# Kernel optimization log

Hardware: AMD Instinct MI355X
Metric: run time of the kernel (lower is better)

The kernel has to match this reference:

```python
import jax, jax.numpy as jnp
import numpy as np

B, S_WP, D_BERT = 64, 512, 768
NUM_WORDS = 256   # max words per sentence (segment count for scatter-mean)
H = 256           # LSTM hidden dim
A_MAX, K_MAX = 8, 4
N_LABELS = 4


def setup_inputs() -> dict:
    key = jax.random.key(0)
    ks = jax.random.split(key, 16)
    s = lambda shape, k, scale=0.05: jax.random.normal(k, shape, jnp.float32) * scale
    inp = {
        "embeddings": jax.random.normal(ks[0], (B, S_WP, D_BERT), jnp.float32),
        "mask": jnp.sort(jax.random.randint(ks[1], (B, S_WP), 0, NUM_WORDS), axis=-1),
        "aspect_idxs": jax.random.randint(ks[2], (B, A_MAX, K_MAX), 0, NUM_WORDS - 2),
        "w_ih_f": s((4 * H, D_BERT), ks[3]),
        "w_hh_f": s((4 * H, H), ks[4]),
        "b_ih_f": s((4 * H,), ks[5]),
        "b_hh_f": s((4 * H,), ks[6]),
        "w_ih_r": s((4 * H, D_BERT), ks[7]),
        "w_hh_r": s((4 * H, H), ks[8]),
        "b_ih_r": s((4 * H,), ks[9]),
        "b_hh_r": s((4 * H,), ks[10]),
        "fc1_w": s((H, 4 * H), ks[11]),
        "fc1_b": s((H,), ks[12]),
        "fc2_w": s((N_LABELS, H), ks[13]),
        "fc2_b": s((N_LABELS,), ks[14]),
    }
    return inp


def _lstm_dir(x, w_ih, w_hh, b_ih, b_hh, reverse):
    # x: [B, S, D] -> [B, S, H]; PyTorch gate order i, f, g, o.
    b, _, _ = x.shape
    h_dim = w_hh.shape[1]
    xg = jnp.einsum('bsd,gd->bsg', x, w_ih) + b_ih  # precompute input gates

    def step(carry, xg_t):
        h, c = carry
        g = xg_t + h @ w_hh.T + b_hh
        i, f, gg, o = jnp.split(g, 4, axis=-1)
        c = jax.nn.sigmoid(f) * c + jax.nn.sigmoid(i) * jnp.tanh(gg)
        h = jax.nn.sigmoid(o) * jnp.tanh(c)
        return (h, c), h

    init = (jnp.zeros((b, h_dim), x.dtype), jnp.zeros((b, h_dim), x.dtype))
    _, hs = jax.lax.scan(step, init, xg.transpose(1, 0, 2), reverse=reverse)
    return hs.transpose(1, 0, 2)


def _forward(embeddings, mask, aspect_idxs, w_ih_f, w_hh_f, b_ih_f, b_hh_f,
             w_ih_r, w_hh_r, b_ih_r, b_hh_r, fc1_w, fc1_b, fc2_w, fc2_b):
    # batch_scatter_mean: pool wordpieces into words via segment mean.
    seg_sum = jax.vmap(lambda e, m: jax.ops.segment_sum(e, m, num_segments=NUM_WORDS))(embeddings, mask)
    cnt = jax.vmap(lambda m: jax.ops.segment_sum(jnp.ones(m.shape, embeddings.dtype), m, num_segments=NUM_WORDS))(mask)
    words = seg_sum / jnp.maximum(cnt, 1.0)[..., None]  # [B, NUM_WORDS, D_BERT]

    # Bidirectional LSTM (dropout is identity in eval).
    h_f = _lstm_dir(words, w_ih_f, w_hh_f, b_ih_f, b_hh_f, reverse=False)
    h_r = _lstm_dir(words, w_ih_r, w_hh_r, b_ih_r, b_hh_r, reverse=True)
    out = jnp.concatenate([h_f, h_r], axis=-1)  # [B, S_words, 2H]

    b, s, hd = out.shape
    sent_mean = out.mean(axis=1)  # [B, 2H] (mean over full padded sequence, as original)

    # Ragged aspect gather-mean: sent_out[idxs + 1].mean(0), -1 pads masked out.
    tok_valid = (aspect_idxs >= 0).astype(out.dtype)              # [B, A, K]
    idx = jnp.clip(aspect_idxs, 0, s - 2) + 1                     # [B, A, K]
    gathered = jnp.take_along_axis(out, idx.reshape(b, -1, 1), axis=1)  # [B, A*K, 2H]
    gathered = gathered.reshape(b, A_MAX, K_MAX, hd)
    n_tok = tok_valid.sum(-1)                                     # [B, A]
    asp_mean = (gathered * tok_valid[..., None]).sum(2) / jnp.maximum(n_tok, 1.0)[..., None]

    valid = (n_tok > 0)[..., None]
    sent_b = jnp.broadcast_to(sent_mean[:, None, :], (b, A_MAX, hd))
    emb = jnp.where(valid, jnp.concatenate([sent_b, asp_mean], axis=-1), 0.0)  # [B, A, 4H]

    flat = emb.reshape(b * A_MAX, 2 * hd)
    h1 = jax.nn.relu(flat @ fc1_w.T + fc1_b)
    logits = h1 @ fc2_w.T + fc2_b
    return logits.reshape(b, A_MAX, -1)


def reference(embeddings, mask, aspect_idxs, w_ih_f, w_hh_f, b_ih_f, b_hh_f,
              w_ih_r, w_hh_r, b_ih_r, b_hh_r, fc1_w, fc1_b, fc2_w, fc2_b):
    return _forward(embeddings, mask, aspect_idxs, w_ih_f, w_hh_f, b_ih_f, b_hh_f,
                    w_ih_r, w_hh_r, b_ih_r, b_hh_r, fc1_w, fc1_b, fc2_w, fc2_b)
```

## Files before the change

### kernel.cpp

```cpp
#include <hip/hip_runtime.h>
#include <hip/hip_bf16.h>
#include <hip/hip_fp16.h>

#define B_   64
#define SWP  512
#define D_   768
#define W_   256
#define H_   256
#define G4   1024
#define N2   2048
#define M_   16384
#define A_   8
#define KK_  4

typedef __attribute__((ext_vector_type(4))) float f32x4;
typedef __attribute__((ext_vector_type(8))) short bf16x8;
typedef _Float16 __attribute__((ext_vector_type(2))) h2_t;

#define KR2 96
#define KT2 32

__device__ __forceinline__ void gload_lds16(const void* g, void* l) {
  __builtin_amdgcn_global_load_lds((const __attribute__((address_space(1))) void*)g,
                                   (__attribute__((address_space(3))) void*)l, 16, 0, 0);
}

__device__ __forceinline__ float sigm(float x) { return 1.f / (1.f + __expf(-x)); }
__device__ __forceinline__ float tanh_(float x) { return 1.f - 2.f / (1.f + __expf(2.f * x)); }

__device__ __forceinline__ float dot2acc(h2_t w, h2_t h, float acc) {
#if __has_builtin(__builtin_amdgcn_fdot2)
  return __builtin_amdgcn_fdot2(w, h, acc, false);
#else
  return acc + (float)w[0] * (float)h[0] + (float)w[1] * (float)h[1];
#endif
}

__device__ __forceinline__ h2_t bc_h2(unsigned int v) {
  union { unsigned int u; h2_t h; } cvt;
  cvt.u = v;
  return cvt.h;
}

__global__ __launch_bounds__(256) void k_words(const float* __restrict__ emb,
                                               const int* __restrict__ mask,
                                               __hip_bfloat16* __restrict__ words) {
  const int b = blockIdx.x >> 8;
  const int w = blockIdx.x & 255;
  const int tid = threadIdx.x;
  __shared__ int m[SWP];
  m[tid] = mask[b * SWP + tid];
  m[tid + 256] = mask[b * SWP + 256 + tid];
  __syncthreads();
  int lo = 0, hi = SWP;
  while (lo < hi) { int mid = (lo + hi) >> 1; if (m[mid] < w) lo = mid + 1; else hi = mid; }
  int lo2 = lo, hi2 = SWP;
  while (lo2 < hi2) { int mid = (lo2 + hi2) >> 1; if (m[mid] < w + 1) lo2 = mid + 1; else hi2 = mid; }
  const int cnt = lo2 - lo;
  const float inv = (cnt > 0) ? 1.f / (float)cnt : 0.f;
  float s0 = 0.f, s1 = 0.f, s2 = 0.f;
  for (int s = lo; s < lo2; ++s) {
    const float* row = emb + ((size_t)b * SWP + s) * D_;
    s0 += row[tid]; s1 += row[tid + 256]; s2 += row[tid + 512];
  }
  __hip_bfloat16* o = words + ((size_t)b * W_ + w) * D_;
  o[tid]       = __float2bfloat16(s0 * inv);
  o[tid + 256] = __float2bfloat16(s1 * inv);
  o[tid + 512] = __float2bfloat16(s2 * inv);
}

__global__ __launch_bounds__(256) void k_prep_wih(const float* __restrict__ wf, const float* __restrict__ wr,
                                                  const float* __restrict__ bihf, const float* __restrict__ bhhf,
                                                  const float* __restrict__ bihr, const float* __restrict__ bhhr,
                                                  __hip_bfloat16* __restrict__ wih, float* __restrict__ bias) {
  const int i = blockIdx.x * 256 + threadIdx.x;
  const int n = i / D_;
  const int k = i - n * D_;
  const float v = (n < G4) ? wf[n * D_ + k] : wr[(n - G4) * D_ + k];
  wih[i] = __float2bfloat16(v);
  if (i < N2) {
    bias[i] = (i < G4) ? (bihf[i] + bhhf[i]) : (bihr[i - G4] + bhhr[i - G4]);
  }
}

__global__ __launch_bounds__(256) void k_prep_whh(const float* __restrict__ whf,
                                                  const float* __restrict__ whr,
                                                  h2_t* __restrict__ whhP) {
  const int i = blockIdx.x * 256 + threadIdx.x;
  const int d = i >> 17;
  const int kk = (i >> 10) & 127;
  const int r = i & 1023;
  const float* w = d ? whr : whf;
  h2_t v;
  v[0] = (_Float16)w[r * H_ + 2 * kk];
  v[1] = (_Float16)w[r * H_ + 2 * kk + 1];
  whhP[i] = v;
}

__global__ __launch_bounds__(256) void k_gemm_xg(const __hip_bfloat16* __restrict__ A,
                                                 const __hip_bfloat16* __restrict__ Wt,
                                                 const float* __restrict__ bias,
                                                 _Float16* __restrict__ C) {
  const int bm = blockIdx.y * 128;
  const int bn = blockIdx.x * 128;
  __shared__ __hip_bfloat16 As[128 * 32];
  __shared__ __hip_bfloat16 Bs[128 * 32];
  const int tid = threadIdx.x;
  const int lane = tid & 63;
  const int wave = tid >> 6;
  const int wm = (wave >> 1) * 64;
  const int wn = (wave & 1) * 64;
  const int l15 = lane & 15;
  const int l4 = lane >> 4;
  const int row_a = tid >> 2;
  const int chunk = tid & 3;
  f32x4 acc[4][4] = {};
  for (int k0 = 0; k0 < D_; k0 += 32) {
    const __hip_bfloat16* ga  = A  + (size_t)(bm + row_a) * D_ + k0 + chunk * 8;
    const __hip_bfloat16* ga2 = A  + (size_t)(bm + 64 + row_a) * D_ + k0 + chunk * 8;
    const __hip_bfloat16* gb  = Wt + (size_t)(bn + row_a) * D_ + k0 + chunk * 8;
    const __hip_bfloat16* gb2 = Wt + (size_t)(bn + 64 + row_a) * D_ + k0 + chunk * 8;
    gload_lds16(ga,  As + tid * 8);
    gload_lds16(ga2, As + 2048 + tid * 8);
    gload_lds16(gb,  Bs + tid * 8);
    gload_lds16(gb2, Bs + 2048 + tid * 8);
    __syncthreads();
    bf16x8 af[4], bf[4];
#pragma unroll
    for (int i = 0; i < 4; ++i) {
      af[i] = *(const bf16x8*)(As + (wm + i * 16 + l15) * 32 + l4 * 8);
      bf[i] = *(const bf16x8*)(Bs + (wn + i * 16 + l15) * 32 + l4 * 8);
    }
#pragma unroll
    for (int i = 0; i < 4; ++i)
#pragma unroll
      for (int j = 0; j < 4; ++j)
        acc[i][j] = __builtin_amdgcn_mfma_f32_16x16x32_bf16(af[i], bf[j], acc[i][j], 0, 0, 0);
    __syncthreads();
  }
#pragma unroll
  for (int i = 0; i < 4; ++i) {
    const int m = bm + wm + i * 16 + l4 * 4;
#pragma unroll
    for (int j = 0; j < 4; ++j) {
      const int n = bn + wn + j * 16 + l15;
      const float bs = bias[n];
#pragma unroll
      for (int r = 0; r < 4; ++r)
        C[(size_t)(m + r) * N2 + n] = (_Float16)(acc[i][j][r] + bs);
    }
  }
}

__global__ __launch_bounds__(1024)
void k_lstm(const _Float16* __restrict__ xg,
            const h2_t* __restrict__ whhP,
            float* __restrict__ out) {
  const int bx = blockIdx.x;
  const int d = bx & 1;
  const int b = bx >> 1;
  const int t = threadIdx.x;
  const int u = t & 255;
  const int gate = t >> 8;
  const int l = t & 63;

  __shared__ __align__(16) _Float16 hbuf[2][256];
  __shared__ __align__(16) h2_t wtail[8][1024][4];
  __shared__ float gbuf[3][256];

  const h2_t* wp = whhP + (size_t)d * (128 * 1024);
  h2_t wreg[KR2];
#pragma unroll
  for (int kk = 0; kk < KR2; ++kk) wreg[kk] = wp[kk * 1024 + t];
#pragma unroll
  for (int c = 0; c < 8; ++c) {
#pragma unroll
    for (int j = 0; j < 4; ++j)
      wtail[c][t][j] = wp[(KR2 + c * 4 + j) * 1024 + t];
  }
  if (t < 256) hbuf[0][t] = (_Float16)0.f;
  __syncthreads();

  float c_state = 0.f;
  for (int step = 0; step < W_; ++step) {
    const int tt = d ? (W_ - 1 - step) : step;
    const float xv = (float)xg[((size_t)b * W_ + tt) * N2 + d * G4 + t];
    const unsigned int hA = *(const unsigned int*)&hbuf[step & 1][2 * l];
    const unsigned int hB = *(const unsigned int*)&hbuf[step & 1][128 + 2 * l];
    float a = 0.f, a2 = 0.f;
#pragma unroll
    for (int kk = 0; kk < 64; kk += 2) {
      a  = dot2acc(wreg[kk],     bc_h2(__builtin_amdgcn_readlane(hA, kk)),     a);
      a2 = dot2acc(wreg[kk + 1], bc_h2(__builtin_amdgcn_readlane(hA, kk + 1)), a2);
    }
#pragma unroll
    for (int kk = 64; kk < KR2; kk += 2) {
      a  = dot2acc(wreg[kk],     bc_h2(__builtin_amdgcn_readlane(hB, kk - 64)),     a);
      a2 = dot2acc(wreg[kk + 1], bc_h2(__builtin_amdgcn_readlane(hB, kk - 63)), a2);
    }
#pragma unroll
    for (int c = 0; c < 8; ++c) {
      const f32x4 wv = *(const f32x4*)&wtail[c][t][0];
      const h2_t* wvp = (const h2_t*)&wv;
      a  = dot2acc(wvp[0], bc_h2(__builtin_amdgcn_readlane(hB, 32 + c * 4 + 0)), a);
      a2 = dot2acc(wvp[1], bc_h2(__builtin_amdgcn_readlane(hB, 32 + c * 4 + 1)), a2);
      a  = dot2acc(wvp[2], bc_h2(__builtin_amdgcn_readlane(hB, 32 + c * 4 + 2)), a);
      a2 = dot2acc(wvp[3], bc_h2(__builtin_amdgcn_readlane(hB, 32 + c * 4 + 3)), a2);
    }
    const float av = a + a2 + xv;
    if (gate != 0) gbuf[gate - 1][u] = av;
    __syncthreads();
    if (gate == 0) {
      const float ig = sigm(av);
      const float fg = sigm(gbuf[0][u]);
      const float gg = tanh_(gbuf[1][u]);
      const float og = sigm(gbuf[2][u]);
      c_state = fg * c_state + ig * gg;
      const float h = og * tanh_(c_state);
      out[((size_t)b * W_ + tt) * 512 + d * 256 + u] = h;
      hbuf[(step + 1) & 1][u] = (_Float16)h;
    }
    __syncthreads();
  }
}

__global__ __launch_bounds__(256) void k_head(const float* __restrict__ out,
                                              const int* __restrict__ aidx,
                                              const float* __restrict__ fc1w,
                                              const float* __restrict__ fc1b,
                                              const float* __restrict__ fc2w,
                                              const float* __restrict__ fc2b,
                                              float* __restrict__ logits) {
  const int b = blockIdx.x;
  const int t = threadIdx.x;
  __shared__ float emb[A_][1024];
  __shared__ float h1[A_][256];
  __shared__ float sent[512];
  const float* ob = out + (size_t)b * W_ * 512;
  float s0 = 0.f, s1 = 0.f;
  for (int tt = 0; tt < W_; ++tt) {
    s0 += ob[tt * 512 + t];
    s1 += ob[tt * 512 + 256 + t];
  }
  sent[t] = s0 * (1.f / 256.f);
  sent[t + 256] = s1 * (1.f / 256.f);
  __syncthreads();
  for (int a = 0; a < A_; ++a) {
    int nv = 0;
    float m0 = 0.f, m1 = 0.f;
    for (int k = 0; k < KK_; ++k) {
      const int idx = aidx[(b * A_ + a) * KK_ + k];
      if (idx >= 0) {
        const int tt = min(idx, W_ - 2) + 1;
        m0 += ob[tt * 512 + t];
        m1 += ob[tt * 512 + 256 + t];
        nv++;
      }
    }
    const float inv = nv > 0 ? 1.f / (float)nv : 0.f;
    const bool valid = nv > 0;
    emb[a][t]        = valid ? sent[t] : 0.f;
    emb[a][t + 256]  = valid ? sent[t + 256] : 0.f;
    emb[a][512 + t]       = m0 * inv;
    emb[a][512 + 256 + t] = m1 * inv;
  }
  __syncthreads();
  {
    float acc[A_];
#pragma unroll
    for (int a = 0; a < A_; ++a) acc[a] = fc1b[t];
    const float* wrow = fc1w + (size_t)t * 1024;
    for (int j = 0; j < 1024; j += 4) {
      const float4 w = *(const float4*)(wrow + j);
#pragma unroll
      for (int a = 0; a < A_; ++a) {
        const float4 e = *(const float4*)(&emb[a][j]);
        acc[a] += w.x * e.x + w.y * e.y + w.z * e.z + w.w * e.w;
      }
    }
#pragma unroll
    for (int a = 0; a < A_; ++a) h1[a][t] = fmaxf(acc[a], 0.f);
  }
  __syncthreads();
  if (t < A_ * 4) {
    const int a = t >> 2, l = t & 3;
    float acc = fc2b[l];
    const float* w = fc2w + l * 256;
    for (int j = 0; j < 256; ++j) acc += w[j] * h1[a][j];
    logits[(b * A_ + a) * 4 + l] = acc;
  }
}

extern "C" void kernel_launch(void* const* d_in, const int* in_sizes, int n_in,
                              void* d_out, int out_size, void* d_ws, size_t ws_size,
                              hipStream_t stream) {
  const float* emb  = (const float*)d_in[0];
  const int*   mask = (const int*)d_in[1];
  const int*   aidx = (const int*)d_in[2];
  const float* wihf = (const float*)d_in[3];
  const float* whhf = (const float*)d_in[4];
  const float* bihf = (const float*)d_in[5];
  const float* bhhf = (const float*)d_in[6];
  const float* wihr = (const float*)d_in[7];
  const float* whhr = (const float*)d_in[8];
  const float* bihr = (const float*)d_in[9];
  const float* bhhr = (const float*)d_in[10];
  const float* fc1w = (const float*)d_in[11];
  const float* fc1b = (const float*)d_in[12];
  const float* fc2w = (const float*)d_in[13];
  const float* fc2b = (const float*)d_in[14];
  float* logits = (float*)d_out;

  char* ws = (char*)d_ws;
  size_t off = 0;
  auto alloc = [&](size_t bytes) -> void* {
    void* p = ws + off;
    off += (bytes + 255) & ~(size_t)255;
    return p;
  };
  __hip_bfloat16* words = (__hip_bfloat16*)alloc((size_t)M_ * D_ * 2);
  _Float16*       xg    = (_Float16*)alloc((size_t)M_ * N2 * 2);
  __hip_bfloat16* wih   = (__hip_bfloat16*)alloc((size_t)N2 * D_ * 2);
  float*          bias  = (float*)alloc((size_t)N2 * 4);
  h2_t*           whhP  = (h2_t*)alloc((size_t)2 * 128 * 1024 * 4);
  float*          outh  = (float*)alloc((size_t)B_ * W_ * 512 * 4);

  k_words<<<B_ * W_, 256, 0, stream>>>(emb, mask, words);
  k_prep_wih<<<(N2 * D_) / 256, 256, 0, stream>>>(wihf, wihr, bihf, bhhf, bihr, bhhr, wih, bias);
  k_prep_whh<<<(2 * 128 * 1024) / 256, 256, 0, stream>>>(whhf, whhr, whhP);
  dim3 gg(N2 / 128, M_ / 128);
  k_gemm_xg<<<gg, 256, 0, stream>>>(words, wih, bias, xg);
  k_lstm<<<B_ * 2, 1024, 0, stream>>>(xg, whhP, outh);
  k_head<<<B_, 256, 0, stream>>>(outh, aidx, fc1w, fc1b, fc2w, fc2b, logits);
}
```

Baseline: 746.1 us.

## Compute all four LSTM gates per thread in 256-thread blocks

The LSTM recurrence kernel moves from 1024 threads (one gate per thread) to 256 threads, each computing all four gates for one hidden unit. This removes the gate-exchange shared buffer and one barrier per step. Hidden state is now read as vectors from LDS instead of broadcast with readlane, and the next step's input gates are prefetched. In exchange each thread holds 384 packed weight registers at one wave per EU, so spilling and reduced latency hiding are risks.

```diff
diff --git a/kernel.cpp b/kernel.cpp
--- a/kernel.cpp
+++ b/kernel.cpp
@@ -34,12 +34,6 @@
 #else
   return acc + (float)w[0] * (float)h[0] + (float)w[1] * (float)h[1];
 #endif
-}
-
-__device__ __forceinline__ h2_t bc_h2(unsigned int v) {
-  union { unsigned int u; h2_t h; } cvt;
-  cvt.u = v;
-  return cvt.h;
 }
 
 __global__ __launch_bounds__(256) void k_words(const float* __restrict__ emb,
@@ -152,7 +146,8 @@
   }
 }
 
-__global__ __launch_bounds__(1024)
+__global__ __launch_bounds__(256)
+__attribute__((amdgpu_waves_per_eu(1, 1)))
 void k_lstm(const _Float16* __restrict__ xg,
             const h2_t* __restrict__ whhP,
             float* __restrict__ out) {
@@ -160,67 +155,97 @@
   const int d = bx & 1;
   const int b = bx >> 1;
   const int t = threadIdx.x;
-  const int u = t & 255;
-  const int gate = t >> 8;
-  const int l = t & 63;
 
   __shared__ __align__(16) _Float16 hbuf[2][256];
-  __shared__ __align__(16) h2_t wtail[8][1024][4];
-  __shared__ float gbuf[3][256];
+  __shared__ __align__(16) h2_t wtail[32][256][4];
 
   const h2_t* wp = whhP + (size_t)d * (128 * 1024);
-  h2_t wreg[KR2];
-#pragma unroll
-  for (int kk = 0; kk < KR2; ++kk) wreg[kk] = wp[kk * 1024 + t];
-#pragma unroll
-  for (int c = 0; c < 8; ++c) {
-#pragma unroll
-    for (int j = 0; j < 4; ++j)
-      wtail[c][t][j] = wp[(KR2 + c * 4 + j) * 1024 + t];
-  }
-  if (t < 256) hbuf[0][t] = (_Float16)0.f;
-  __syncthreads();
+
+  h2_t wI[KR2], wF[KR2], wG[KR2], wO[KR2];
+#pragma unroll 96
+  for (int kk = 0; kk < KR2; ++kk) {
+    wI[kk] = wp[kk * 1024 + t];
+    wF[kk] = wp[kk * 1024 + 256 + t];
+    wG[kk] = wp[kk * 1024 + 512 + t];
+    wO[kk] = wp[kk * 1024 + 768 + t];
+  }
+#pragma unroll
+  for (int c = 0; c < 32; ++c) {
+    const int g = c >> 3, j = c & 7;
+    f32x4 v;
+#pragma unroll
+    for (int q = 0; q < 4; ++q) {
+      h2_t w = wp[(KR2 + j * 4 + q) * 1024 + g * 256 + t];
+      ((h2_t*)&v)[q] = w;
+    }
+    *(f32x4*)&wtail[c][t][0] = v;
+  }
+  hbuf[0][t] = (_Float16)0.f;
+  __syncthreads();
+
+  int tt = d ? (W_ - 1) : 0;
+  const _Float16* xr = xg + ((size_t)b * W_ + tt) * N2 + d * G4;
+  float xI = (float)xr[t], xF = (float)xr[256 + t];
+  float xG = (float)xr[512 + t], xO = (float)xr[768 + t];
 
   float c_state = 0.f;
   for (int step = 0; step < W_; ++step) {
-    const int tt = d ? (W_ - 1 - step) : step;
-    const float xv = (float)xg[((size_t)b * W_ + tt) * N2 + d * G4 + t];
-    const unsigned int hA = *(const unsigned int*)&hbuf[step & 1][2 * l];
-    const unsigned int hB = *(const unsigned int*)&hbuf[step & 1][128 + 2 * l];
-    float a = 0.f, a2 = 0.f;
-#pragma unroll
-    for (int kk = 0; kk < 64; kk += 2) {
-      a  = dot2acc(wreg[kk],     bc_h2(__builtin_amdgcn_readlane(hA, kk)),     a);
-      a2 = dot2acc(wreg[kk + 1], bc_h2(__builtin_amdgcn_readlane(hA, kk + 1)), a2);
-    }
-#pragma unroll
-    for (int kk = 64; kk < KR2; kk += 2) {
-      a  = dot2acc(wreg[kk],     bc_h2(__builtin_amdgcn_readlane(hB, kk - 64)),     a);
-      a2 = dot2acc(wreg[kk + 1], bc_h2(__builtin_amdgcn_readlane(hB, kk - 63)), a2);
-    }
-#pragma unroll
-    for (int c = 0; c < 8; ++c) {
-      const f32x4 wv = *(const f32x4*)&wtail[c][t][0];
-      const h2_t* wvp = (const h2_t*)&wv;
-      a  = dot2acc(wvp[0], bc_h2(__builtin_amdgcn_readlane(hB, 32 + c * 4 + 0)), a);
-      a2 = dot2acc(wvp[1], bc_h2(__builtin_amdgcn_readlane(hB, 32 + c * 4 + 1)), a2);
-      a  = dot2acc(wvp[2], bc_h2(__builtin_amdgcn_readlane(hB, 32 + c * 4 + 2)), a);
-      a2 = dot2acc(wvp[3], bc_h2(__builtin_amdgcn_readlane(hB, 32 + c * 4 + 3)), a2);
-    }
-    const float av = a + a2 + xv;
-    if (gate != 0) gbuf[gate - 1][u] = av;
+    const int cur = step & 1;
+    float nI = 0.f, nF = 0.f, nG = 0.f, nO = 0.f;
+    if (step + 1 < W_) {
+      const int tt1 = d ? (W_ - 2 - step) : (step + 1);
+      const _Float16* xr1 = xg + ((size_t)b * W_ + tt1) * N2 + d * G4;
+      nI = (float)xr1[t]; nF = (float)xr1[256 + t];
+      nG = (float)xr1[512 + t]; nO = (float)xr1[768 + t];
+    }
+
+    const f32x4* hb4 = (const f32x4*)&hbuf[cur][0];
+    float aI = 0.f, aF = 0.f, aG = 0.f, aO = 0.f;
+#pragma unroll
+    for (int c = 0; c < 24; ++c) {
+      const f32x4 hv = hb4[c];
+      const h2_t* hp = (const h2_t*)&hv;
+#pragma unroll
+      for (int q = 0; q < 4; ++q) {
+        aI = dot2acc(wI[c * 4 + q], hp[q], aI);
+        aF = dot2acc(wF[c * 4 + q], hp[q], aF);
+        aG = dot2acc(wG[c * 4 + q], hp[q], aG);
+        aO = dot2acc(wO[c * 4 + q], hp[q], aO);
+      }
+    }
+#pragma unroll
+    for (int j = 0; j < 8; ++j) {
+      const f32x4 hv = hb4[24 + j];
+      const h2_t* hp = (const h2_t*)&hv;
+      const f32x4 vI = *(const f32x4*)&wtail[j][t][0];
+      const f32x4 vF = *(const f32x4*)&wtail[8 + j][t][0];
+      const f32x4 vG = *(const f32x4*)&wtail[16 + j][t][0];
+      const f32x4 vO = *(const f32x4*)&wtail[24 + j][t][0];
+      const h2_t* pI = (const h2_t*)&vI;
+      const h2_t* pF = (const h2_t*)&vF;
+      const h2_t* pG = (const h2_t*)&vG;
+      const h2_t* pO = (const h2_t*)&vO;
+#pragma unroll
+      for (int q = 0; q < 4; ++q) {
+        aI = dot2acc(pI[q], hp[q], aI);
+        aF = dot2acc(pF[q], hp[q], aF);
+        aG = dot2acc(pG[q], hp[q], aG);
+        aO = dot2acc(pO[q], hp[q], aO);
+      }
+    }
+
+    const float ig = sigm(aI + xI);
+    const float fg = sigm(aF + xF);
+    const float gg = tanh_(aG + xG);
+    const float og = sigm(aO + xO);
+    c_state = fg * c_state + ig * gg;
+    const float h = og * tanh_(c_state);
+    out[((size_t)b * W_ + tt) * 512 + d * 256 + t] = h;
+    hbuf[cur ^ 1][t] = (_Float16)h;
     __syncthreads();
-    if (gate == 0) {
-      const float ig = sigm(av);
-      const float fg = sigm(gbuf[0][u]);
-      const float gg = tanh_(gbuf[1][u]);
-      const float og = sigm(gbuf[2][u]);
-      c_state = fg * c_state + ig * gg;
-      const float h = og * tanh_(c_state);
-      out[((size_t)b * W_ + tt) * 512 + d * 256 + u] = h;
-      hbuf[(step + 1) & 1][u] = (_Float16)h;
-    }
-    __syncthreads();
+
+    tt = d ? (W_ - 2 - step) : (step + 1);
+    xI = nI; xF = nF; xG = nG; xO = nO;
   }
 }
 
@@ -330,6 +355,6 @@
   k_prep_whh<<<(2 * 128 * 1024) / 256, 256, 0, stream>>>(whhf, whhr, whhP);
   dim3 gg(N2 / 128, M_ / 128);
   k_gemm_xg<<<gg, 256, 0, stream>>>(words, wih, bias, xg);
-  k_lstm<<<B_ * 2, 1024, 0, stream>>>(xg, whhP, outh);
+  k_lstm<<<B_ * 2, 256, 0, stream>>>(xg, whhP, outh);
   k_head<<<B_, 256, 0, stream>>>(outh, aidx, fc1w, fc1b, fc2w, fc2b, logits);
 }
```

Result: slower. 1.030 ms (+38.1%).

## Split each LSTM sequence across two workgroups with flag-based hidden-state exchange

Applied to the files above, without the earlier changes.

The recurrent LSTM kernel now uses two 512-thread workgroups per (batch, direction) pair, each owning half the hidden units. After every step the halves swap their fp16 hidden vectors through global memory, using release/acquire flags and spin-waiting. The recurrent weights are spread over registers, LDS and a pre-packed global stream that is reloaded every step. This doubles the number of CUs working on the serial recurrence, at the cost of a cross-workgroup handshake per timestep that assumes all 256 workgroups are co-resident.

```diff
diff --git a/kernel.cpp b/kernel.cpp
--- a/kernel.cpp
+++ b/kernel.cpp
@@ -17,8 +17,9 @@
 typedef __attribute__((ext_vector_type(8))) short bf16x8;
 typedef _Float16 __attribute__((ext_vector_type(2))) h2_t;
 
-#define KR2 96
-#define KT2 32
+#define PVC 32
+#define NLC 12
+#define NSC 12
 
 __device__ __forceinline__ void gload_lds16(const void* g, void* l) {
   __builtin_amdgcn_global_load_lds((const __attribute__((address_space(1))) void*)g,
@@ -95,6 +96,28 @@
   v[0] = (_Float16)w[r * H_ + 2 * kk];
   v[1] = (_Float16)w[r * H_ + 2 * kk + 1];
   whhP[i] = v;
+}
+
+__global__ __launch_bounds__(256) void k_prep_wstr(const h2_t* __restrict__ whhP,
+                                                   f32x4* __restrict__ wstr) {
+  const int i = blockIdx.x * 256 + threadIdx.x;
+  if (i >= 2 * 2 * NSC * 512) return;
+  const int t = i & 511;
+  const int c = (i >> 9) % NSC;
+  const int duh = i / (NSC * 512);
+  const int d = duh >> 1;
+  const int uh = duh & 1;
+  const int r = (t >> 7) * 256 + uh * 128 + (t & 127);
+  const h2_t* wp = whhP + (size_t)d * (128 * 1024);
+  f32x4 v;
+#pragma unroll
+  for (int q = 0; q < 4; ++q)
+    ((h2_t*)&v)[q] = wp[(80 + 4 * c + q) * 1024 + r];
+  wstr[i] = v;
+}
+
+__global__ __launch_bounds__(256) void k_zero_flags(int* __restrict__ flags) {
+  flags[threadIdx.x] = 0;
 }
 
 __global__ __launch_bounds__(256) void k_gemm_xg(const __hip_bfloat16* __restrict__ A,
@@ -152,75 +175,126 @@
   }
 }
 
-__global__ __launch_bounds__(1024)
+__global__ __launch_bounds__(512)
 void k_lstm(const _Float16* __restrict__ xg,
             const h2_t* __restrict__ whhP,
+            const f32x4* __restrict__ wstr,
+            unsigned* __restrict__ hx,
+            int* __restrict__ flags,
             float* __restrict__ out) {
-  const int bx = blockIdx.x;
-  const int d = bx & 1;
-  const int b = bx >> 1;
+  const int bid = blockIdx.x;
+  const int p = bid & 127;
+  const int uh = bid >> 7;
+  const int d = p & 1;
+  const int b = p >> 1;
   const int t = threadIdx.x;
-  const int u = t & 255;
-  const int gate = t >> 8;
+  const int g = t >> 7;
+  const int us = t & 127;
+  const int u = uh * 128 + us;
+  const int r = g * 256 + u;
   const int l = t & 63;
-
-  __shared__ __align__(16) _Float16 hbuf[2][256];
-  __shared__ __align__(16) h2_t wtail[8][1024][4];
-  __shared__ float gbuf[3][256];
+  const int myidx = p * 2 + uh;
+  const int paidx = p * 2 + (uh ^ 1);
+
+  __shared__ __align__(16) _Float16 hbuf[256];
+  __shared__ __align__(16) h2_t wlds[NLC][512][4];
+  __shared__ float gbuf[3][128];
 
   const h2_t* wp = whhP + (size_t)d * (128 * 1024);
-  h2_t wreg[KR2];
-#pragma unroll
-  for (int kk = 0; kk < KR2; ++kk) wreg[kk] = wp[kk * 1024 + t];
-#pragma unroll
-  for (int c = 0; c < 8; ++c) {
-#pragma unroll
-    for (int j = 0; j < 4; ++j)
-      wtail[c][t][j] = wp[(KR2 + c * 4 + j) * 1024 + t];
-  }
-  if (t < 256) hbuf[0][t] = (_Float16)0.f;
+  const f32x4* wsp = wstr + (size_t)(d * 2 + uh) * (NSC * 512);
+
+  unsigned wv[PVC];
+#pragma unroll
+  for (int j = 0; j < PVC; ++j)
+    wv[j] = *(const unsigned*)&wp[j * 1024 + r];
+#pragma unroll
+  for (int c = 0; c < NLC; ++c) {
+    f32x4 v;
+#pragma unroll
+    for (int q = 0; q < 4; ++q)
+      ((h2_t*)&v)[q] = wp[(PVC + 4 * c + q) * 1024 + r];
+    *(f32x4*)&wlds[c][t][0] = v;
+  }
+  if (t < 256) hbuf[t] = (_Float16)0.f;
   __syncthreads();
 
   float c_state = 0.f;
+#pragma unroll 1
   for (int step = 0; step < W_; ++step) {
     const int tt = d ? (W_ - 1 - step) : step;
-    const float xv = (float)xg[((size_t)b * W_ + tt) * N2 + d * G4 + t];
-    const unsigned int hA = *(const unsigned int*)&hbuf[step & 1][2 * l];
-    const unsigned int hB = *(const unsigned int*)&hbuf[step & 1][128 + 2 * l];
+    const float xv = (float)xg[((size_t)b * W_ + tt) * N2 + d * G4 + r];
     float a = 0.f, a2 = 0.f;
-#pragma unroll
-    for (int kk = 0; kk < 64; kk += 2) {
-      a  = dot2acc(wreg[kk],     bc_h2(__builtin_amdgcn_readlane(hA, kk)),     a);
-      a2 = dot2acc(wreg[kk + 1], bc_h2(__builtin_amdgcn_readlane(hA, kk + 1)), a2);
-    }
-#pragma unroll
-    for (int kk = 64; kk < KR2; kk += 2) {
-      a  = dot2acc(wreg[kk],     bc_h2(__builtin_amdgcn_readlane(hB, kk - 64)),     a);
-      a2 = dot2acc(wreg[kk + 1], bc_h2(__builtin_amdgcn_readlane(hB, kk - 63)), a2);
-    }
-#pragma unroll
-    for (int c = 0; c < 8; ++c) {
-      const f32x4 wv = *(const f32x4*)&wtail[c][t][0];
-      const h2_t* wvp = (const h2_t*)&wv;
-      a  = dot2acc(wvp[0], bc_h2(__builtin_amdgcn_readlane(hB, 32 + c * 4 + 0)), a);
-      a2 = dot2acc(wvp[1], bc_h2(__builtin_amdgcn_readlane(hB, 32 + c * 4 + 1)), a2);
-      a  = dot2acc(wvp[2], bc_h2(__builtin_amdgcn_readlane(hB, 32 + c * 4 + 2)), a);
-      a2 = dot2acc(wvp[3], bc_h2(__builtin_amdgcn_readlane(hB, 32 + c * 4 + 3)), a2);
+    if (step > 0) {
+      f32x4 sw[NSC];
+#pragma unroll
+      for (int c = 0; c < NSC; ++c) sw[c] = wsp[c * 512 + t];
+      const unsigned hA = *(const unsigned*)&hbuf[2 * l];
+      const unsigned hB = *(const unsigned*)&hbuf[128 + 2 * l];
+#pragma unroll
+      for (int j = 0; j < PVC; ++j) {
+        const h2_t hq = bc_h2(__builtin_amdgcn_readlane(hA, j));
+        if (j & 1) a2 = dot2acc(bc_h2(wv[j]), hq, a2);
+        else       a  = dot2acc(bc_h2(wv[j]), hq, a);
+      }
+#pragma unroll
+      for (int c = 0; c < NLC; ++c) {
+        const f32x4 wchunk = *(const f32x4*)&wlds[c][t][0];
+        const h2_t* wc = (const h2_t*)&wchunk;
+#pragma unroll
+        for (int q = 0; q < 4; ++q) {
+          const int pp = PVC + 4 * c + q;
+          const h2_t hq = bc_h2((pp < 64) ? __builtin_amdgcn_readlane(hA, pp)
+                                          : __builtin_amdgcn_readlane(hB, pp - 64));
+          if (q & 1) a2 = dot2acc(wc[q], hq, a2);
+          else       a  = dot2acc(wc[q], hq, a);
+        }
+      }
+#pragma unroll
+      for (int c = 0; c < NSC; ++c) {
+        const h2_t* wc = (const h2_t*)&sw[c];
+#pragma unroll
+        for (int q = 0; q < 4; ++q) {
+          const int pp = 80 + 4 * c + q;
+          const h2_t hq = bc_h2(__builtin_amdgcn_readlane(hB, pp - 64));
+          if (q & 1) a2 = dot2acc(wc[q], hq, a2);
+          else       a  = dot2acc(wc[q], hq, a);
+        }
+      }
     }
     const float av = a + a2 + xv;
-    if (gate != 0) gbuf[gate - 1][u] = av;
+    if (g) gbuf[g - 1][us] = av;
     __syncthreads();
-    if (gate == 0) {
+    if (!g) {
       const float ig = sigm(av);
-      const float fg = sigm(gbuf[0][u]);
-      const float gg = tanh_(gbuf[1][u]);
-      const float og = sigm(gbuf[2][u]);
+      const float fg = sigm(gbuf[0][us]);
+      const float gg = tanh_(gbuf[1][us]);
+      const float og = sigm(gbuf[2][us]);
       c_state = fg * c_state + ig * gg;
       const float h = og * tanh_(c_state);
       out[((size_t)b * W_ + tt) * 512 + d * 256 + u] = h;
-      hbuf[(step + 1) & 1][u] = (_Float16)h;
+      hbuf[u] = (_Float16)h;
     }
     __syncthreads();
+    if (step < W_ - 1) {
+      if (t < 64) {
+        const unsigned pk = *(const unsigned*)&hbuf[uh * 128 + 2 * l];
+        __hip_atomic_store(&hx[myidx * 64 + l], pk, __ATOMIC_RELAXED,
+                           __HIP_MEMORY_SCOPE_AGENT);
+        __threadfence();
+        if (t == 0)
+          __hip_atomic_store(&flags[myidx], step + 1, __ATOMIC_RELEASE,
+                             __HIP_MEMORY_SCOPE_AGENT);
+        int v;
+        do {
+          v = __hip_atomic_load(&flags[paidx], __ATOMIC_ACQUIRE,
+                                __HIP_MEMORY_SCOPE_AGENT);
+        } while (v <= step);
+        const unsigned pk2 = __hip_atomic_load(&hx[paidx * 64 + l], __ATOMIC_RELAXED,
+                                               __HIP_MEMORY_SCOPE_AGENT);
+        *(unsigned*)&hbuf[(uh ^ 1) * 128 + 2 * l] = pk2;
+      }
+      __syncthreads();
+    }
   }
 }
 
@@ -323,13 +397,18 @@
   __hip_bfloat16* wih   = (__hip_bfloat16*)alloc((size_t)N2 * D_ * 2);
   float*          bias  = (float*)alloc((size_t)N2 * 4);
   h2_t*           whhP  = (h2_t*)alloc((size_t)2 * 128 * 1024 * 4);
+  f32x4*          wstr  = (f32x4*)alloc((size_t)2 * 2 * NSC * 512 * 16);
+  unsigned*       hx    = (unsigned*)alloc((size_t)256 * 64 * 4);
+  int*            flg   = (int*)alloc((size_t)256 * 4);
   float*          outh  = (float*)alloc((size_t)B_ * W_ * 512 * 4);
 
   k_words<<<B_ * W_, 256, 0, stream>>>(emb, mask, words);
   k_prep_wih<<<(N2 * D_) / 256, 256, 0, stream>>>(wihf, wihr, bihf, bhhf, bihr, bhhr, wih, bias);
   k_prep_whh<<<(2 * 128 * 1024) / 256, 256, 0, stream>>>(whhf, whhr, whhP);
+  k_prep_wstr<<<(2 * 2 * NSC * 512 + 255) / 256, 256, 0, stream>>>(whhP, wstr);
+  k_zero_flags<<<1, 256, 0, stream>>>(flg);
   dim3 gg(N2 / 128, M_ / 128);
   k_gemm_xg<<<gg, 256, 0, stream>>>(words, wih, bias, xg);
-  k_lstm<<<B_ * 2, 1024, 0, stream>>>(xg, whhP, outh);
+  k_lstm<<<256, 512, 0, stream>>>(xg, whhP, wstr, hx, flg, outh);
   k_head<<<B_, 256, 0, stream>>>(outh, aidx, fc1w, fc1b, fc2w, fc2b, logits);
 }
```

After: 2.755 ms. 3.69x slower.
